# Kernel optimization log

Measured on AMD Instinct MI355X. Metric: run time of the kernel, lower is better.

## Reference

```python
import jax, jax.numpy as jnp
import numpy as np

N, EMB, ATT = 65536, 1024, 512


def setup_inputs() -> dict:
    key = jax.random.key(0)
    k = jax.random.split(key, 6)
    scale = 0.02
    return {
        "leaves": jax.random.normal(k[0], (N, EMB), dtype=jnp.float32),
        "ancestors": jax.random.normal(k[1], (N, EMB), dtype=jnp.float32),
        "W1": jax.random.normal(k[2], (2 * EMB, ATT), dtype=jnp.float32) * scale,
        "b1": jax.random.normal(k[3], (ATT,), dtype=jnp.float32) * scale,
        "W2": jax.random.normal(k[4], (ATT, 1), dtype=jnp.float32) * scale,
        "b2": jax.random.normal(k[5], (1,), dtype=jnp.float32) * scale,
    }


def reference(leaves, ancestors, W1, b1, W2, b2):
    # concat -> [N, 2*EMB]
    x = jnp.concatenate([leaves, ancestors], axis=-1)
    # additive attention MLP: linear -> tanh -> linear -> [N, 1]
    h = jnp.tanh(x @ W1 + b1)
    scores = h @ W2 + b2            # [N, 1]
    attn = jax.nn.softmax(scores, axis=0)  # softmax over the pair dim
    # reshape to [1, N], matmul ancestors [N, EMB] -> [1, EMB], sum dim 0 -> [EMB]
    out = jnp.squeeze(attn, axis=1) @ ancestors  # [EMB]
    return out
```

## Files before the change

kernel.cpp:

```cpp
#include <hip/hip_runtime.h>
#include <hip/hip_bf16.h>
#include <stdint.h>
#include <stddef.h>

typedef __bf16 bf16;
typedef bf16 bf16x8 __attribute__((ext_vector_type(8)));
typedef bf16 bf16x4 __attribute__((ext_vector_type(4)));
typedef float f32x4 __attribute__((ext_vector_type(4)));

#define N_ROWS 65536
#define EMB    1024
#define ATTD   512
#define KDIM   2048
#define BM     128
#define BK     64
#define NBLK   (N_ROWS / BM)

__device__ __forceinline__ void gload_lds16(const void* g, void* l) {
  __builtin_amdgcn_global_load_lds(
      (const __attribute__((address_space(1))) void*)g,
      (__attribute__((address_space(3))) void*)l, 16, 0, 0);
}

__global__ __launch_bounds__(256) void k_prep_w1(const float* __restrict__ W1,
                                                 bf16* __restrict__ W1t) {
  __shared__ float tile[64][65];
  const int bx = blockIdx.x;
  const int by = blockIdx.y;
  const int t  = threadIdx.x;
  const int k0 = bx * 64, n0 = by * 64;

  const int kt = t >> 2, c4 = (t & 3) * 16;
  const float* src = W1 + (size_t)(k0 + kt) * ATTD + n0 + c4;
  #pragma unroll
  for (int q = 0; q < 4; q++) {
    float4 v = *(const float4*)(src + q * 4);
    tile[kt][c4 + q * 4 + 0] = v.x;
    tile[kt][c4 + q * 4 + 1] = v.y;
    tile[kt][c4 + q * 4 + 2] = v.z;
    tile[kt][c4 + q * 4 + 3] = v.w;
  }
  __syncthreads();

  const int nr = t >> 2;
  const int n_glob = n0 + nr;
  const size_t base = (size_t)n_glob * KDIM + k0;
  #pragma unroll
  for (int h = 0; h < 2; h++) {
    const int ktbase = c4 + h * 8;
    bf16x8 o;
    #pragma unroll
    for (int e = 0; e < 8; e++) o[e] = (bf16)tile[ktbase + e][nr];
    const int chunk = ((ktbase >> 3) ^ (n_glob & 7));
    *(bf16x8*)(W1t + base + chunk * 8) = o;
  }
}

__global__ __launch_bounds__(512) void k_gemm_score(
    const float* __restrict__ leaves, const float* __restrict__ anc,
    const bf16* __restrict__ W1t, const float* __restrict__ b1,
    const float* __restrict__ W2, const float* __restrict__ b2,
    float* __restrict__ scores, float* __restrict__ bmax,
    float* __restrict__ bsum) {
  __shared__ bf16 ldsA[BM * BK];
  __shared__ bf16 ldsB[ATTD * BK];

  const int t    = threadIdx.x;
  const int lane = t & 63;
  const int wave = t >> 6;
  const int l15  = lane & 15;
  const int l4   = lane >> 4;
  const int wm   = wave >> 2;
  const int wn   = wave & 3;
  const int m0   = blockIdx.x * BM;

  const f32x4 zero4 = {0.f, 0.f, 0.f, 0.f};
  f32x4 acc[4][8];
  #pragma unroll
  for (int i = 0; i < 4; i++)
    #pragma unroll
    for (int j = 0; j < 8; j++) acc[i][j] = zero4;

  for (int kb = 0; kb < KDIM / BK; kb++) {
    const float* Abase = (kb < 16)
        ? (leaves + (size_t)m0 * EMB + (size_t)kb * BK)
        : (anc    + (size_t)m0 * EMB + (size_t)(kb - 16) * BK);
    #pragma unroll
    for (int s = 0; s < 4; s++) {
      const int i  = s * 512 + t;
      const int r  = i >> 4;
      const int c4 = i & 15;
      float4 v = *(const float4*)(Abase + (size_t)r * EMB + c4 * 4);
      bf16x4 o = {(bf16)v.x, (bf16)v.y, (bf16)v.z, (bf16)v.w};
      const int chunk = (c4 >> 1) ^ (r & 7);
      *(bf16x4*)(ldsA + r * BK + chunk * 8 + (c4 & 1) * 4) = o;
    }
    #pragma unroll
    for (int c = 0; c < 8; c++) {
      const int chunkid = (wave * 8 + c) * 64 + lane;
      const int nr = chunkid >> 3;
      const int cc = chunkid & 7;
      gload_lds16(W1t + (size_t)nr * KDIM + kb * BK + cc * 8,
                  ldsB + (wave * 8 + c) * 512);
    }
    __syncthreads();
    #pragma unroll
    for (int ks = 0; ks < 2; ks++) {
      bf16x8 afr[4];
      #pragma unroll
      for (int mi = 0; mi < 4; mi++) {
        const int row   = wm * 64 + mi * 16 + l15;
        const int chunk = (ks * 4 + l4) ^ (row & 7);
        afr[mi] = *(const bf16x8*)(ldsA + row * BK + chunk * 8);
      }
      #pragma unroll
      for (int ni = 0; ni < 8; ni++) {
        const int nrow  = wn * 128 + ni * 16 + l15;
        const int chunk = (ks * 4 + l4) ^ (nrow & 7);
        bf16x8 bfr = *(const bf16x8*)(ldsB + nrow * BK + chunk * 8);
        #pragma unroll
        for (int mi = 0; mi < 4; mi++)
          acc[mi][ni] = __builtin_amdgcn_mfma_f32_16x16x32_bf16(
              afr[mi], bfr, acc[mi][ni], 0, 0, 0);
      }
    }
    __syncthreads();
  }

  float b1c[8], w2c[8];
  #pragma unroll
  for (int ni = 0; ni < 8; ni++) {
    const int col = wn * 128 + ni * 16 + l15;
    b1c[ni] = b1[col];
    w2c[ni] = W2[col];
  }
  float* sp   = (float*)ldsA;
  float* redm = sp + 512;
  float* redz = sp + 520;
  #pragma unroll
  for (int mi = 0; mi < 4; mi++) {
    #pragma unroll
    for (int r = 0; r < 4; r++) {
      float p = 0.f;
      #pragma unroll
      for (int ni = 0; ni < 8; ni++)
        p += tanhf(acc[mi][ni][r] + b1c[ni]) * w2c[ni];
      p += __shfl_xor(p, 1);
      p += __shfl_xor(p, 2);
      p += __shfl_xor(p, 4);
      p += __shfl_xor(p, 8);
      if (l15 == 0) sp[wn * 128 + wm * 64 + mi * 16 + l4 * 4 + r] = p;
    }
  }
  __syncthreads();
  float myscore = 0.f;
  if (t < BM) {
    myscore = sp[t] + sp[128 + t] + sp[256 + t] + sp[384 + t] + b2[0];
    scores[m0 + t] = myscore;
  }
  float mm = (t < BM) ? myscore : -3.0e38f;
  #pragma unroll
  for (int o = 32; o; o >>= 1) mm = fmaxf(mm, __shfl_xor(mm, o));
  if (lane == 0) redm[wave] = mm;
  __syncthreads();
  if (t == 0) {
    float g = redm[0];
    for (int i = 1; i < 8; i++) g = fmaxf(g, redm[i]);
    redm[0] = g;
  }
  __syncthreads();
  const float bM = redm[0];
  float ee = (t < BM) ? __expf(myscore - bM) : 0.f;
  #pragma unroll
  for (int o = 32; o; o >>= 1) ee += __shfl_xor(ee, o);
  if (lane == 0) redz[wave] = ee;
  __syncthreads();
  if (t == 0) {
    float z = 0.f;
    for (int i = 0; i < 8; i++) z += redz[i];
    bmax[blockIdx.x] = bM;
    bsum[blockIdx.x] = z;
  }
}

__global__ __launch_bounds__(512) void k_mz(const float* __restrict__ bmax,
                                            const float* __restrict__ bsum,
                                            float* __restrict__ MZ) {
  const int t = threadIdx.x, lane = t & 63, wave = t >> 6;
  __shared__ float rm[8], rs[8];
  const float m = bmax[t];
  float mm = m;
  #pragma unroll
  for (int o = 32; o; o >>= 1) mm = fmaxf(mm, __shfl_xor(mm, o));
  if (lane == 0) rm[wave] = mm;
  __syncthreads();
  if (t == 0) {
    float g = rm[0];
    for (int i = 1; i < 8; i++) g = fmaxf(g, rm[i]);
    rm[0] = g;
  }
  __syncthreads();
  const float M = rm[0];
  float z = bsum[t] * __expf(m - M);
  #pragma unroll
  for (int o = 32; o; o >>= 1) z += __shfl_xor(z, o);
  if (lane == 0) rs[wave] = z;
  __syncthreads();
  if (t == 0) {
    float Z = 0.f;
    for (int i = 0; i < 8; i++) Z += rs[i];
    MZ[0] = M;
    MZ[1] = Z;
  }
}

__global__ __launch_bounds__(256) void k_part(const float* __restrict__ anc,
                                              const float* __restrict__ scores,
                                              const float* __restrict__ MZ,
                                              float* __restrict__ part) {
  __shared__ float w[BM];
  const int b = blockIdx.x, t = threadIdx.x;
  const float M = MZ[0];
  if (t < BM) w[t] = __expf(scores[(size_t)b * BM + t] - M);
  __syncthreads();
  float4 a = {0.f, 0.f, 0.f, 0.f};
  const float4* src = (const float4*)(anc + (size_t)b * BM * EMB) + t;
  #pragma unroll 4
  for (int i = 0; i < BM; i++) {
    float4 v = src[i * (EMB / 4)];
    const float wi = w[i];
    a.x += wi * v.x;
    a.y += wi * v.y;
    a.z += wi * v.z;
    a.w += wi * v.w;
  }
  ((float4*)(part + (size_t)b * EMB))[t] = a;
}

__global__ __launch_bounds__(256) void k_final(const float* __restrict__ part,
                                               const float* __restrict__ MZ,
                                               float* __restrict__ out) {
  const int j = blockIdx.x * 256 + threadIdx.x;
  float s0 = 0.f, s1 = 0.f, s2 = 0.f, s3 = 0.f;
  for (int b = 0; b < NBLK; b += 4) {
    s0 += part[(size_t)(b + 0) * EMB + j];
    s1 += part[(size_t)(b + 1) * EMB + j];
    s2 += part[(size_t)(b + 2) * EMB + j];
    s3 += part[(size_t)(b + 3) * EMB + j];
  }
  out[j] = (s0 + s1 + s2 + s3) / MZ[1];
}

extern "C" void kernel_launch(void* const* d_in, const int* in_sizes, int n_in,
                              void* d_out, int out_size, void* d_ws,
                              size_t ws_size, hipStream_t stream) {
  const float* leaves = (const float*)d_in[0];
  const float* anc    = (const float*)d_in[1];
  const float* W1     = (const float*)d_in[2];
  const float* b1     = (const float*)d_in[3];
  const float* W2     = (const float*)d_in[4];
  const float* b2     = (const float*)d_in[5];
  float* out = (float*)d_out;

  char* ws = (char*)d_ws;
  bf16*  W1t    = (bf16*)ws;
  float* scores = (float*)(ws + (1u << 21));
  float* bmax   = (float*)(ws + (1u << 21) + (1u << 18));
  float* bsum   = bmax + NBLK;
  float* MZ     = bsum + NBLK;
  float* part   = (float*)(ws + (1u << 21) + (1u << 19));

  k_prep_w1<<<dim3(32, 8), 256, 0, stream>>>(W1, W1t);
  k_gemm_score<<<dim3(NBLK), 512, 0, stream>>>(leaves, anc, W1t, b1, W2, b2,
                                               scores, bmax, bsum);
  k_mz<<<dim3(1), 512, 0, stream>>>(bmax, bsum, MZ);
  k_part<<<dim3(NBLK), 256, 0, stream>>>(anc, scores, MZ, part);
  k_final<<<dim3(EMB / 256), 256, 0, stream>>>(part, MZ, out);
}
```

Baseline: 337.6 us.

## Double-buffer GEMM LDS tiles with BK=32 and K-block-major W1 layout

Splits the K dimension into 32-wide blocks and double-buffers both A and B tiles in LDS. The next block's global loads are issued before the current MFMAs, so memory latency can overlap with compute and one barrier per iteration is dropped. The W1 prep kernel now writes a contiguous K-block-major layout with a new XOR swizzle. The trade-off is twice as many loop iterations with less MFMA work per barrier, plus extra registers held live during prefetch.

```diff
diff --git a/kernel.cpp b/kernel.cpp
--- a/kernel.cpp
+++ b/kernel.cpp
@@ -13,7 +13,8 @@
 #define ATTD   512
 #define KDIM   2048
 #define BM     128
-#define BK     64
+#define BK     32
+#define NKB    (KDIM / BK)
 #define NBLK   (N_ROWS / BM)
 
 __device__ __forceinline__ void gload_lds16(const void* g, void* l) {
@@ -24,36 +25,31 @@
 
 __global__ __launch_bounds__(256) void k_prep_w1(const float* __restrict__ W1,
                                                  bf16* __restrict__ W1t) {
-  __shared__ float tile[64][65];
-  const int bx = blockIdx.x;
-  const int by = blockIdx.y;
+  __shared__ float tile[32][72];
+  const int kb = blockIdx.x;
+  const int ng = blockIdx.y;
   const int t  = threadIdx.x;
-  const int k0 = bx * 64, n0 = by * 64;
-
-  const int kt = t >> 2, c4 = (t & 3) * 16;
-  const float* src = W1 + (size_t)(k0 + kt) * ATTD + n0 + c4;
-  #pragma unroll
-  for (int q = 0; q < 4; q++) {
-    float4 v = *(const float4*)(src + q * 4);
-    tile[kt][c4 + q * 4 + 0] = v.x;
-    tile[kt][c4 + q * 4 + 1] = v.y;
-    tile[kt][c4 + q * 4 + 2] = v.z;
-    tile[kt][c4 + q * 4 + 3] = v.w;
-  }
-  __syncthreads();
-
-  const int nr = t >> 2;
-  const int n_glob = n0 + nr;
-  const size_t base = (size_t)n_glob * KDIM + k0;
-  #pragma unroll
-  for (int h = 0; h < 2; h++) {
-    const int ktbase = c4 + h * 8;
-    bf16x8 o;
-    #pragma unroll
-    for (int e = 0; e < 8; e++) o[e] = (bf16)tile[ktbase + e][nr];
-    const int chunk = ((ktbase >> 3) ^ (n_glob & 7));
-    *(bf16x8*)(W1t + base + chunk * 8) = o;
-  }
+  const int n0 = ng * 64;
+
+  const int kr  = t >> 3;
+  const int nc8 = (t & 7) * 8;
+  const float* src = W1 + (size_t)(kb * 32 + kr) * ATTD + n0 + nc8;
+  float4 v0 = *(const float4*)(src);
+  float4 v1 = *(const float4*)(src + 4);
+  tile[kr][nc8 + 0] = v0.x; tile[kr][nc8 + 1] = v0.y;
+  tile[kr][nc8 + 2] = v0.z; tile[kr][nc8 + 3] = v0.w;
+  tile[kr][nc8 + 4] = v1.x; tile[kr][nc8 + 5] = v1.y;
+  tile[kr][nc8 + 6] = v1.z; tile[kr][nc8 + 7] = v1.w;
+  __syncthreads();
+
+  const int nl = t >> 2;
+  const int p  = t & 3;
+  const int n  = n0 + nl;
+  const int c  = p ^ ((n >> 1) & 3);
+  bf16x8 o;
+  #pragma unroll
+  for (int e = 0; e < 8; e++) o[e] = (bf16)tile[c * 8 + e][nl];
+  *(bf16x8*)(W1t + (size_t)kb * (ATTD * BK) + (size_t)n * 32 + p * 8) = o;
 }
 
 __global__ __launch_bounds__(512) void k_gemm_score(
@@ -62,8 +58,8 @@
     const float* __restrict__ W2, const float* __restrict__ b2,
     float* __restrict__ scores, float* __restrict__ bmax,
     float* __restrict__ bsum) {
-  __shared__ bf16 ldsA[BM * BK];
-  __shared__ bf16 ldsB[ATTD * BK];
+  __shared__ bf16 ldsA[2][BM * BK];
+  __shared__ bf16 ldsB[2][ATTD * BK];
 
   const int t    = threadIdx.x;
   const int lane = t & 63;
@@ -74,6 +70,11 @@
   const int wn   = wave & 3;
   const int m0   = blockIdx.x * BM;
 
+  const int ar = t >> 2;
+  const int ac = t & 3;
+  const int apc = ac ^ ((ar >> 1) & 3);
+  const int a_lds_off = ar * BK + apc * 8;
+
   const f32x4 zero4 = {0.f, 0.f, 0.f, 0.f};
   f32x4 acc[4][8];
   #pragma unroll
@@ -81,48 +82,66 @@
     #pragma unroll
     for (int j = 0; j < 8; j++) acc[i][j] = zero4;
 
-  for (int kb = 0; kb < KDIM / BK; kb++) {
-    const float* Abase = (kb < 16)
-        ? (leaves + (size_t)m0 * EMB + (size_t)kb * BK)
-        : (anc    + (size_t)m0 * EMB + (size_t)(kb - 16) * BK);
-    #pragma unroll
-    for (int s = 0; s < 4; s++) {
-      const int i  = s * 512 + t;
-      const int r  = i >> 4;
-      const int c4 = i & 15;
-      float4 v = *(const float4*)(Abase + (size_t)r * EMB + c4 * 4);
-      bf16x4 o = {(bf16)v.x, (bf16)v.y, (bf16)v.z, (bf16)v.w};
-      const int chunk = (c4 >> 1) ^ (r & 7);
-      *(bf16x4*)(ldsA + r * BK + chunk * 8 + (c4 & 1) * 4) = o;
-    }
-    #pragma unroll
-    for (int c = 0; c < 8; c++) {
-      const int chunkid = (wave * 8 + c) * 64 + lane;
-      const int nr = chunkid >> 3;
-      const int cc = chunkid & 7;
-      gload_lds16(W1t + (size_t)nr * KDIM + kb * BK + cc * 8,
-                  ldsB + (wave * 8 + c) * 512);
-    }
+  int a_rd[4];
+  #pragma unroll
+  for (int mi = 0; mi < 4; mi++) {
+    const int row = wm * 64 + mi * 16 + l15;
+    a_rd[mi] = row * BK + (l4 ^ ((row >> 1) & 3)) * 8;
+  }
+  int b_rd[8];
+  #pragma unroll
+  for (int ni = 0; ni < 8; ni++) {
+    const int nrow = wn * 128 + ni * 16 + l15;
+    b_rd[ni] = nrow * BK + (l4 ^ ((nrow >> 1) & 3)) * 8;
+  }
+
+  {
+    const float* Abase = leaves + (size_t)m0 * EMB;
+    float4 v0 = *(const float4*)(Abase + (size_t)ar * EMB + ac * 8);
+    float4 v1 = *(const float4*)(Abase + (size_t)ar * EMB + ac * 8 + 4);
+    #pragma unroll
+    for (int j = 0; j < 4; j++)
+      gload_lds16(W1t + ((size_t)(wave * 4 + j) * 64 + lane) * 8,
+                  &ldsB[0][(wave * 4 + j) * 512]);
+    bf16x8 o = {(bf16)v0.x, (bf16)v0.y, (bf16)v0.z, (bf16)v0.w,
+                (bf16)v1.x, (bf16)v1.y, (bf16)v1.z, (bf16)v1.w};
+    *(bf16x8*)(&ldsA[0][a_lds_off]) = o;
     __syncthreads();
-    #pragma unroll
-    for (int ks = 0; ks < 2; ks++) {
-      bf16x8 afr[4];
+  }
+
+  for (int kb = 0; kb < NKB; kb++) {
+    const int cur = kb & 1, nxt = cur ^ 1;
+    float4 v0, v1;
+    const bool pf = (kb < NKB - 1);
+    if (pf) {
+      const int kn = kb + 1;
+      const float* Abase = (kn < 32)
+          ? (leaves + (size_t)m0 * EMB + (size_t)kn * BK)
+          : (anc    + (size_t)m0 * EMB + (size_t)(kn - 32) * BK);
+      v0 = *(const float4*)(Abase + (size_t)ar * EMB + ac * 8);
+      v1 = *(const float4*)(Abase + (size_t)ar * EMB + ac * 8 + 4);
+      const bf16* Bsrc = W1t + (size_t)kn * (ATTD * BK);
       #pragma unroll
-      for (int mi = 0; mi < 4; mi++) {
-        const int row   = wm * 64 + mi * 16 + l15;
-        const int chunk = (ks * 4 + l4) ^ (row & 7);
-        afr[mi] = *(const bf16x8*)(ldsA + row * BK + chunk * 8);
-      }
+      for (int j = 0; j < 4; j++)
+        gload_lds16(Bsrc + ((size_t)(wave * 4 + j) * 64 + lane) * 8,
+                    &ldsB[nxt][(wave * 4 + j) * 512]);
+    }
+    bf16x8 afr[4];
+    #pragma unroll
+    for (int mi = 0; mi < 4; mi++)
+      afr[mi] = *(const bf16x8*)(&ldsA[cur][a_rd[mi]]);
+    #pragma unroll
+    for (int ni = 0; ni < 8; ni++) {
+      bf16x8 bfr = *(const bf16x8*)(&ldsB[cur][b_rd[ni]]);
       #pragma unroll
-      for (int ni = 0; ni < 8; ni++) {
-        const int nrow  = wn * 128 + ni * 16 + l15;
-        const int chunk = (ks * 4 + l4) ^ (nrow & 7);
-        bf16x8 bfr = *(const bf16x8*)(ldsB + nrow * BK + chunk * 8);
-        #pragma unroll
-        for (int mi = 0; mi < 4; mi++)
-          acc[mi][ni] = __builtin_amdgcn_mfma_f32_16x16x32_bf16(
-              afr[mi], bfr, acc[mi][ni], 0, 0, 0);
-      }
+      for (int mi = 0; mi < 4; mi++)
+        acc[mi][ni] = __builtin_amdgcn_mfma_f32_16x16x32_bf16(
+            afr[mi], bfr, acc[mi][ni], 0, 0, 0);
+    }
+    if (pf) {
+      bf16x8 o = {(bf16)v0.x, (bf16)v0.y, (bf16)v0.z, (bf16)v0.w,
+                  (bf16)v1.x, (bf16)v1.y, (bf16)v1.z, (bf16)v1.w};
+      *(bf16x8*)(&ldsA[nxt][a_lds_off]) = o;
     }
     __syncthreads();
   }
@@ -134,7 +153,7 @@
     b1c[ni] = b1[col];
     w2c[ni] = W2[col];
   }
-  float* sp   = (float*)ldsA;
+  float* sp   = (float*)&ldsA[0][0];
   float* redm = sp + 512;
   float* redz = sp + 520;
   #pragma unroll
@@ -270,7 +289,7 @@
   float* MZ     = bsum + NBLK;
   float* part   = (float*)(ws + (1u << 21) + (1u << 19));
 
-  k_prep_w1<<<dim3(32, 8), 256, 0, stream>>>(W1, W1t);
+  k_prep_w1<<<dim3(64, 8), 256, 0, stream>>>(W1, W1t);
   k_gemm_score<<<dim3(NBLK), 512, 0, stream>>>(leaves, anc, W1t, b1, W2, b2,
                                                scores, bmax, bsum);
   k_mz<<<dim3(1), 512, 0, stream>>>(bmax, bsum, MZ);
```

Measured after the change: 361.2 us. 7.0% more time.

## Double-buffer GEMM LDS tiles with register-prefetched A and k-block-major W1 layout

Applied to the files above, without the earlier changes.

Reworks the score GEMM into a software pipeline: LDS A and B tiles are double-buffered, A for k-block kb+2 is prefetched into registers while block kb computes, and W1 for the next block is streamed via global_load_lds into the alternate buffer, with a single manual waitcnt+barrier per step instead of two syncthreads. W1t is re-laid out k-block-major so each block's B tile is one contiguous 64KB chunk. Launch bounds request 2 blocks per CU. This trades doubled LDS (160KB per block) and higher register pressure for overlap of loads with MFMA; LDS size may actually limit occupancy to one block.

```diff
diff --git a/kernel.cpp b/kernel.cpp
--- a/kernel.cpp
+++ b/kernel.cpp
@@ -5,7 +5,6 @@
 
 typedef __bf16 bf16;
 typedef bf16 bf16x8 __attribute__((ext_vector_type(8)));
-typedef bf16 bf16x4 __attribute__((ext_vector_type(4)));
 typedef float f32x4 __attribute__((ext_vector_type(4)));
 
 #define N_ROWS 65536
@@ -14,6 +13,7 @@
 #define KDIM   2048
 #define BM     128
 #define BK     64
+#define NKB    (KDIM / BK)
 #define NBLK   (N_ROWS / BM)
 
 __device__ __forceinline__ void gload_lds16(const void* g, void* l) {
@@ -24,46 +24,46 @@
 
 __global__ __launch_bounds__(256) void k_prep_w1(const float* __restrict__ W1,
                                                  bf16* __restrict__ W1t) {
-  __shared__ float tile[64][65];
-  const int bx = blockIdx.x;
-  const int by = blockIdx.y;
+  __shared__ float tile[64][72];
+  const int kb = blockIdx.x;
+  const int ng = blockIdx.y;
   const int t  = threadIdx.x;
-  const int k0 = bx * 64, n0 = by * 64;
-
-  const int kt = t >> 2, c4 = (t & 3) * 16;
-  const float* src = W1 + (size_t)(k0 + kt) * ATTD + n0 + c4;
-  #pragma unroll
-  for (int q = 0; q < 4; q++) {
+  const int n0 = ng * 64;
+
+  const int kr = t >> 2;
+  const int nc = (t & 3) * 16;
+  const float* src = W1 + (size_t)(kb * 64 + kr) * ATTD + n0 + nc;
+  #pragma unroll
+  for (int q = 0; q < 4; ++q) {
     float4 v = *(const float4*)(src + q * 4);
-    tile[kt][c4 + q * 4 + 0] = v.x;
-    tile[kt][c4 + q * 4 + 1] = v.y;
-    tile[kt][c4 + q * 4 + 2] = v.z;
-    tile[kt][c4 + q * 4 + 3] = v.w;
-  }
-  __syncthreads();
-
-  const int nr = t >> 2;
-  const int n_glob = n0 + nr;
-  const size_t base = (size_t)n_glob * KDIM + k0;
-  #pragma unroll
-  for (int h = 0; h < 2; h++) {
-    const int ktbase = c4 + h * 8;
+    tile[kr][nc + q * 4 + 0] = v.x;
+    tile[kr][nc + q * 4 + 1] = v.y;
+    tile[kr][nc + q * 4 + 2] = v.z;
+    tile[kr][nc + q * 4 + 3] = v.w;
+  }
+  __syncthreads();
+
+  const int nl = t >> 2;
+  const int n  = n0 + nl;
+  #pragma unroll
+  for (int h = 0; h < 2; ++h) {
+    const int p = (t & 3) + h * 4;
+    const int c = p ^ (n & 7);
     bf16x8 o;
     #pragma unroll
-    for (int e = 0; e < 8; e++) o[e] = (bf16)tile[ktbase + e][nr];
-    const int chunk = ((ktbase >> 3) ^ (n_glob & 7));
-    *(bf16x8*)(W1t + base + chunk * 8) = o;
-  }
-}
-
-__global__ __launch_bounds__(512) void k_gemm_score(
+    for (int e = 0; e < 8; ++e) o[e] = (bf16)tile[c * 8 + e][nl];
+    *(bf16x8*)(W1t + (size_t)kb * (ATTD * BK) + ((size_t)n * 8 + p) * 8) = o;
+  }
+}
+
+__global__ __launch_bounds__(512, 2) void k_gemm_score(
     const float* __restrict__ leaves, const float* __restrict__ anc,
     const bf16* __restrict__ W1t, const float* __restrict__ b1,
     const float* __restrict__ W2, const float* __restrict__ b2,
     float* __restrict__ scores, float* __restrict__ bmax,
     float* __restrict__ bsum) {
-  __shared__ bf16 ldsA[BM * BK];
-  __shared__ bf16 ldsB[ATTD * BK];
+  __shared__ bf16 ldsA[2][BM * BK];
+  __shared__ bf16 ldsB[2][ATTD * BK];
 
   const int t    = threadIdx.x;
   const int lane = t & 63;
@@ -74,76 +74,132 @@
   const int wn   = wave & 3;
   const int m0   = blockIdx.x * BM;
 
+  const int ar  = t >> 2;
+  const int acb = (t & 3) * 2;
+
   const f32x4 zero4 = {0.f, 0.f, 0.f, 0.f};
   f32x4 acc[4][8];
   #pragma unroll
-  for (int i = 0; i < 4; i++)
+  for (int i = 0; i < 4; ++i)
     #pragma unroll
-    for (int j = 0; j < 8; j++) acc[i][j] = zero4;
-
-  for (int kb = 0; kb < KDIM / BK; kb++) {
-    const float* Abase = (kb < 16)
-        ? (leaves + (size_t)m0 * EMB + (size_t)kb * BK)
-        : (anc    + (size_t)m0 * EMB + (size_t)(kb - 16) * BK);
+    for (int j = 0; j < 8; ++j) acc[i][j] = zero4;
+
+  float4 rA0[4], rA1[4];
+
+  {
+    const float* Ap0 = leaves + (size_t)(m0 + ar) * EMB + acb * 8;
+    rA0[0] = *(const float4*)(Ap0 + 0);
+    rA0[1] = *(const float4*)(Ap0 + 4);
+    rA0[2] = *(const float4*)(Ap0 + 8);
+    rA0[3] = *(const float4*)(Ap0 + 12);
     #pragma unroll
-    for (int s = 0; s < 4; s++) {
-      const int i  = s * 512 + t;
-      const int r  = i >> 4;
-      const int c4 = i & 15;
-      float4 v = *(const float4*)(Abase + (size_t)r * EMB + c4 * 4);
-      bf16x4 o = {(bf16)v.x, (bf16)v.y, (bf16)v.z, (bf16)v.w};
-      const int chunk = (c4 >> 1) ^ (r & 7);
-      *(bf16x4*)(ldsA + r * BK + chunk * 8 + (c4 & 1) * 4) = o;
-    }
-    #pragma unroll
-    for (int c = 0; c < 8; c++) {
-      const int chunkid = (wave * 8 + c) * 64 + lane;
-      const int nr = chunkid >> 3;
-      const int cc = chunkid & 7;
-      gload_lds16(W1t + (size_t)nr * KDIM + kb * BK + cc * 8,
-                  ldsB + (wave * 8 + c) * 512);
-    }
-    __syncthreads();
-    #pragma unroll
-    for (int ks = 0; ks < 2; ks++) {
-      bf16x8 afr[4];
-      #pragma unroll
-      for (int mi = 0; mi < 4; mi++) {
-        const int row   = wm * 64 + mi * 16 + l15;
-        const int chunk = (ks * 4 + l4) ^ (row & 7);
-        afr[mi] = *(const bf16x8*)(ldsA + row * BK + chunk * 8);
-      }
-      #pragma unroll
-      for (int ni = 0; ni < 8; ni++) {
-        const int nrow  = wn * 128 + ni * 16 + l15;
-        const int chunk = (ks * 4 + l4) ^ (nrow & 7);
-        bf16x8 bfr = *(const bf16x8*)(ldsB + nrow * BK + chunk * 8);
-        #pragma unroll
-        for (int mi = 0; mi < 4; mi++)
-          acc[mi][ni] = __builtin_amdgcn_mfma_f32_16x16x32_bf16(
-              afr[mi], bfr, acc[mi][ni], 0, 0, 0);
-      }
-    }
-    __syncthreads();
-  }
+    for (int j = 0; j < 8; ++j)
+      gload_lds16(W1t + ((size_t)(wave * 8 + j) * 64 + lane) * 8,
+                  &ldsB[0][(wave * 8 + j) * 512]);
+    const float* Ap1 = leaves + (size_t)(m0 + ar) * EMB + BK + acb * 8;
+    rA1[0] = *(const float4*)(Ap1 + 0);
+    rA1[1] = *(const float4*)(Ap1 + 4);
+    rA1[2] = *(const float4*)(Ap1 + 8);
+    rA1[3] = *(const float4*)(Ap1 + 12);
+    __builtin_amdgcn_sched_barrier(0);
+    bf16x8 o0 = {(bf16)rA0[0].x, (bf16)rA0[0].y, (bf16)rA0[0].z, (bf16)rA0[0].w,
+                 (bf16)rA0[1].x, (bf16)rA0[1].y, (bf16)rA0[1].z, (bf16)rA0[1].w};
+    bf16x8 o1 = {(bf16)rA0[2].x, (bf16)rA0[2].y, (bf16)rA0[2].z, (bf16)rA0[2].w,
+                 (bf16)rA0[3].x, (bf16)rA0[3].y, (bf16)rA0[3].z, (bf16)rA0[3].w};
+    *(bf16x8*)(&ldsA[0][ar * BK + ((acb + 0) ^ (ar & 7)) * 8]) = o0;
+    *(bf16x8*)(&ldsA[0][ar * BK + ((acb + 1) ^ (ar & 7)) * 8]) = o1;
+    asm volatile("s_waitcnt vmcnt(4) lgkmcnt(0)" ::: "memory");
+    __builtin_amdgcn_s_barrier();
+  }
+
+#define GEMM_BODY(KB, CUR, RISS, RWR, DOSTAGE, DOAISS)                         \
+  do {                                                                         \
+    if (DOSTAGE) {                                                             \
+      const bf16* Bsrc_ = W1t + (size_t)((KB) + 1) * (ATTD * BK);              \
+      _Pragma("unroll")                                                        \
+      for (int j = 0; j < 8; ++j)                                              \
+        gload_lds16(Bsrc_ + ((size_t)(wave * 8 + j) * 64 + lane) * 8,          \
+                    &ldsB[(CUR) ^ 1][(wave * 8 + j) * 512]);                   \
+      if (DOAISS) {                                                            \
+        const int kn_ = (KB) + 2;                                              \
+        const float* Ap_ = (kn_ < 16)                                          \
+            ? leaves + (size_t)(m0 + ar) * EMB + (size_t)kn_ * BK + acb * 8    \
+            : anc + (size_t)(m0 + ar) * EMB + (size_t)(kn_ - 16) * BK + acb * 8;\
+        RISS[0] = *(const float4*)(Ap_ + 0);                                   \
+        RISS[1] = *(const float4*)(Ap_ + 4);                                   \
+        RISS[2] = *(const float4*)(Ap_ + 8);                                   \
+        RISS[3] = *(const float4*)(Ap_ + 12);                                  \
+      }                                                                        \
+      __builtin_amdgcn_sched_barrier(0);                                       \
+    }                                                                          \
+    _Pragma("unroll")                                                          \
+    for (int ks = 0; ks < 2; ++ks) {                                           \
+      bf16x8 af_[4], bf_[8];                                                   \
+      _Pragma("unroll")                                                        \
+      for (int mi = 0; mi < 4; ++mi) {                                         \
+        const int row_ = wm * 64 + mi * 16 + l15;                              \
+        const int p_   = (ks * 4 + l4) ^ (row_ & 7);                           \
+        af_[mi] = *(const bf16x8*)(&ldsA[CUR][row_ * BK + p_ * 8]);            \
+      }                                                                        \
+      _Pragma("unroll")                                                        \
+      for (int ni = 0; ni < 8; ++ni) {                                         \
+        const int nrow_ = wn * 128 + ni * 16 + l15;                            \
+        const int p_    = (ks * 4 + l4) ^ (nrow_ & 7);                         \
+        bf_[ni] = *(const bf16x8*)(&ldsB[CUR][nrow_ * BK + p_ * 8]);           \
+      }                                                                        \
+      _Pragma("unroll")                                                        \
+      for (int ni = 0; ni < 8; ++ni)                                           \
+        _Pragma("unroll")                                                      \
+        for (int mi = 0; mi < 4; ++mi)                                         \
+          acc[mi][ni] = __builtin_amdgcn_mfma_f32_16x16x32_bf16(               \
+              af_[mi], bf_[ni], acc[mi][ni], 0, 0, 0);                         \
+    }                                                                          \
+    if (DOSTAGE) {                                                             \
+      bf16x8 w0_ = {(bf16)RWR[0].x, (bf16)RWR[0].y, (bf16)RWR[0].z,            \
+                    (bf16)RWR[0].w, (bf16)RWR[1].x, (bf16)RWR[1].y,            \
+                    (bf16)RWR[1].z, (bf16)RWR[1].w};                           \
+      bf16x8 w1_ = {(bf16)RWR[2].x, (bf16)RWR[2].y, (bf16)RWR[2].z,            \
+                    (bf16)RWR[2].w, (bf16)RWR[3].x, (bf16)RWR[3].y,            \
+                    (bf16)RWR[3].z, (bf16)RWR[3].w};                           \
+      *(bf16x8*)(&ldsA[(CUR) ^ 1][ar * BK + ((acb + 0) ^ (ar & 7)) * 8]) = w0_;\
+      *(bf16x8*)(&ldsA[(CUR) ^ 1][ar * BK + ((acb + 1) ^ (ar & 7)) * 8]) = w1_;\
+      if (DOAISS) {                                                            \
+        asm volatile("s_waitcnt vmcnt(4) lgkmcnt(0)" ::: "memory");            \
+      } else {                                                                 \
+        asm volatile("s_waitcnt vmcnt(0) lgkmcnt(0)" ::: "memory");            \
+      }                                                                        \
+    } else {                                                                   \
+      asm volatile("s_waitcnt lgkmcnt(0)" ::: "memory");                       \
+    }                                                                          \
+    __builtin_amdgcn_s_barrier();                                              \
+  } while (0)
+
+  for (int kbp = 0; kbp < 15; ++kbp) {
+    const int kb = kbp * 2;
+    GEMM_BODY(kb,     0, rA0, rA1, true, true);
+    GEMM_BODY(kb + 1, 1, rA1, rA0, true, true);
+  }
+  GEMM_BODY(30, 0, rA0, rA1, true,  false);
+  GEMM_BODY(31, 1, rA0, rA1, false, false);
+#undef GEMM_BODY
 
   float b1c[8], w2c[8];
   #pragma unroll
-  for (int ni = 0; ni < 8; ni++) {
+  for (int ni = 0; ni < 8; ++ni) {
     const int col = wn * 128 + ni * 16 + l15;
     b1c[ni] = b1[col];
     w2c[ni] = W2[col];
   }
-  float* sp   = (float*)ldsA;
+  float* sp   = (float*)&ldsA[0][0];
   float* redm = sp + 512;
   float* redz = sp + 520;
   #pragma unroll
-  for (int mi = 0; mi < 4; mi++) {
+  for (int mi = 0; mi < 4; ++mi) {
     #pragma unroll
-    for (int r = 0; r < 4; r++) {
+    for (int r = 0; r < 4; ++r) {
       float p = 0.f;
       #pragma unroll
-      for (int ni = 0; ni < 8; ni++)
+      for (int ni = 0; ni < 8; ++ni)
         p += tanhf(acc[mi][ni][r] + b1c[ni]) * w2c[ni];
       p += __shfl_xor(p, 1);
       p += __shfl_xor(p, 2);
@@ -165,7 +221,7 @@
   __syncthreads();
   if (t == 0) {
     float g = redm[0];
-    for (int i = 1; i < 8; i++) g = fmaxf(g, redm[i]);
+    for (int i = 1; i < 8; ++i) g = fmaxf(g, redm[i]);
     redm[0] = g;
   }
   __syncthreads();
@@ -177,7 +233,7 @@
   __syncthreads();
   if (t == 0) {
     float z = 0.f;
-    for (int i = 0; i < 8; i++) z += redz[i];
+    for (int i = 0; i < 8; ++i) z += redz[i];
     bmax[blockIdx.x] = bM;
     bsum[blockIdx.x] = z;
   }
@@ -196,7 +252,7 @@
   __syncthreads();
   if (t == 0) {
     float g = rm[0];
-    for (int i = 1; i < 8; i++) g = fmaxf(g, rm[i]);
+    for (int i = 1; i < 8; ++i) g = fmaxf(g, rm[i]);
     rm[0] = g;
   }
   __syncthreads();
@@ -208,7 +264,7 @@
   __syncthreads();
   if (t == 0) {
     float Z = 0.f;
-    for (int i = 0; i < 8; i++) Z += rs[i];
+    for (int i = 0; i < 8; ++i) Z += rs[i];
     MZ[0] = M;
     MZ[1] = Z;
   }
@@ -226,7 +282,7 @@
   float4 a = {0.f, 0.f, 0.f, 0.f};
   const float4* src = (const float4*)(anc + (size_t)b * BM * EMB) + t;
   #pragma unroll 4
-  for (int i = 0; i < BM; i++) {
+  for (int i = 0; i < BM; ++i) {
     float4 v = src[i * (EMB / 4)];
     const float wi = w[i];
     a.x += wi * v.x;
```

Result: slower. 505.8 us (+49.8%).

## Split GEMM over N into 128-wide tiles and reorganize softmax reduction pipeline

Applied to the files above, without the earlier changes.

The GEMM block now covers 128x128 tiles with 256 threads instead of 128x512 with 512 threads, so there are four times as many blocks and more can be resident at once. W1 is pre-packed into contiguous per-tile bf16 blocks so the B loads into LDS are contiguous. Partial scores from the four N-splits are written out and summed in a new combine kernel. k_part now weights with per-block maxima and k_final rescales each block, so k_part no longer waits on the global max. The cost is that each A tile (fp32 activations) is read and converted four times, once per N-split.

```diff
diff --git a/kernel.cpp b/kernel.cpp
--- a/kernel.cpp
+++ b/kernel.cpp
@@ -5,7 +5,6 @@
 
 typedef __bf16 bf16;
 typedef bf16 bf16x8 __attribute__((ext_vector_type(8)));
-typedef bf16 bf16x4 __attribute__((ext_vector_type(4)));
 typedef float f32x4 __attribute__((ext_vector_type(4)));
 
 #define N_ROWS 65536
@@ -13,8 +12,11 @@
 #define ATTD   512
 #define KDIM   2048
 #define BM     128
+#define BN     128
 #define BK     64
-#define NBLK   (N_ROWS / BM)
+#define NKB    (KDIM / BK)
+#define MBLK   (N_ROWS / BM)
+#define NSPL   (ATTD / BN)
 
 __device__ __forceinline__ void gload_lds16(const void* g, void* l) {
   __builtin_amdgcn_global_load_lds(
@@ -24,168 +26,186 @@
 
 __global__ __launch_bounds__(256) void k_prep_w1(const float* __restrict__ W1,
                                                  bf16* __restrict__ W1t) {
-  __shared__ float tile[64][65];
-  const int bx = blockIdx.x;
-  const int by = blockIdx.y;
+  __shared__ float tile[64][132];
+  const int kb = blockIdx.x;
+  const int bn = blockIdx.y;
   const int t  = threadIdx.x;
-  const int k0 = bx * 64, n0 = by * 64;
-
-  const int kt = t >> 2, c4 = (t & 3) * 16;
-  const float* src = W1 + (size_t)(k0 + kt) * ATTD + n0 + c4;
-  #pragma unroll
-  for (int q = 0; q < 4; q++) {
+
+  const int kr = t >> 2;
+  const int nc = (t & 3) * 32;
+  const float* src = W1 + (size_t)(kb * 64 + kr) * ATTD + bn * 128 + nc;
+  #pragma unroll
+  for (int q = 0; q < 8; ++q) {
     float4 v = *(const float4*)(src + q * 4);
-    tile[kt][c4 + q * 4 + 0] = v.x;
-    tile[kt][c4 + q * 4 + 1] = v.y;
-    tile[kt][c4 + q * 4 + 2] = v.z;
-    tile[kt][c4 + q * 4 + 3] = v.w;
-  }
-  __syncthreads();
-
-  const int nr = t >> 2;
-  const int n_glob = n0 + nr;
-  const size_t base = (size_t)n_glob * KDIM + k0;
-  #pragma unroll
-  for (int h = 0; h < 2; h++) {
-    const int ktbase = c4 + h * 8;
+    tile[kr][nc + q * 4 + 0] = v.x;
+    tile[kr][nc + q * 4 + 1] = v.y;
+    tile[kr][nc + q * 4 + 2] = v.z;
+    tile[kr][nc + q * 4 + 3] = v.w;
+  }
+  __syncthreads();
+
+  const int nl = t >> 1;
+  const int pb = (t & 1) * 4;
+  bf16* dst = W1t + (size_t)(kb * 4 + bn) * (BN * BK);
+  #pragma unroll
+  for (int pi = 0; pi < 4; ++pi) {
+    const int p = pb + pi;
+    const int c = p ^ (nl & 7);
     bf16x8 o;
     #pragma unroll
-    for (int e = 0; e < 8; e++) o[e] = (bf16)tile[ktbase + e][nr];
-    const int chunk = ((ktbase >> 3) ^ (n_glob & 7));
-    *(bf16x8*)(W1t + base + chunk * 8) = o;
-  }
-}
-
-__global__ __launch_bounds__(512) void k_gemm_score(
+    for (int e = 0; e < 8; ++e) o[e] = (bf16)tile[c * 8 + e][nl];
+    *(bf16x8*)(dst + ((size_t)nl * 8 + p) * 8) = o;
+  }
+}
+
+__global__ __launch_bounds__(256, 3) void k_gemm_score(
     const float* __restrict__ leaves, const float* __restrict__ anc,
     const bf16* __restrict__ W1t, const float* __restrict__ b1,
-    const float* __restrict__ W2, const float* __restrict__ b2,
-    float* __restrict__ scores, float* __restrict__ bmax,
-    float* __restrict__ bsum) {
+    const float* __restrict__ W2, float* __restrict__ spart) {
   __shared__ bf16 ldsA[BM * BK];
-  __shared__ bf16 ldsB[ATTD * BK];
+  __shared__ bf16 ldsB[BN * BK];
 
   const int t    = threadIdx.x;
   const int lane = t & 63;
   const int wave = t >> 6;
   const int l15  = lane & 15;
   const int l4   = lane >> 4;
-  const int wm   = wave >> 2;
-  const int wn   = wave & 3;
-  const int m0   = blockIdx.x * BM;
+  const int wm2  = wave >> 1;
+  const int wn2  = wave & 1;
+  const int bn   = blockIdx.x & 3;
+  const int bm   = blockIdx.x >> 2;
+  const int m0   = bm * BM;
+  const int n0   = bn * BN;
+
+  const int ar   = t >> 1;
+  const int half = t & 1;
 
   const f32x4 zero4 = {0.f, 0.f, 0.f, 0.f};
-  f32x4 acc[4][8];
-  #pragma unroll
-  for (int i = 0; i < 4; i++)
-    #pragma unroll
-    for (int j = 0; j < 8; j++) acc[i][j] = zero4;
-
-  for (int kb = 0; kb < KDIM / BK; kb++) {
-    const float* Abase = (kb < 16)
-        ? (leaves + (size_t)m0 * EMB + (size_t)kb * BK)
-        : (anc    + (size_t)m0 * EMB + (size_t)(kb - 16) * BK);
-    #pragma unroll
-    for (int s = 0; s < 4; s++) {
-      const int i  = s * 512 + t;
-      const int r  = i >> 4;
-      const int c4 = i & 15;
-      float4 v = *(const float4*)(Abase + (size_t)r * EMB + c4 * 4);
-      bf16x4 o = {(bf16)v.x, (bf16)v.y, (bf16)v.z, (bf16)v.w};
-      const int chunk = (c4 >> 1) ^ (r & 7);
-      *(bf16x4*)(ldsA + r * BK + chunk * 8 + (c4 & 1) * 4) = o;
-    }
-    #pragma unroll
-    for (int c = 0; c < 8; c++) {
-      const int chunkid = (wave * 8 + c) * 64 + lane;
-      const int nr = chunkid >> 3;
-      const int cc = chunkid & 7;
-      gload_lds16(W1t + (size_t)nr * KDIM + kb * BK + cc * 8,
-                  ldsB + (wave * 8 + c) * 512);
+  f32x4 acc[4][4];
+  #pragma unroll
+  for (int i = 0; i < 4; ++i)
+    #pragma unroll
+    for (int j = 0; j < 4; ++j) acc[i][j] = zero4;
+
+  for (int kb = 0; kb < NKB; ++kb) {
+    const bf16* Bsrc = W1t + (size_t)(kb * 4 + bn) * (BN * BK);
+    #pragma unroll
+    for (int j = 0; j < 4; ++j)
+      gload_lds16(Bsrc + ((size_t)(wave * 4 + j) * 64 + lane) * 8,
+                  ldsB + (wave * 4 + j) * 512);
+    const float* Ap = ((kb < 16)
+        ? leaves + (size_t)(m0 + ar) * EMB + (size_t)kb * BK
+        : anc    + (size_t)(m0 + ar) * EMB + (size_t)(kb - 16) * BK)
+        + half * 32;
+    float4 v0 = *(const float4*)(Ap + 0);
+    float4 v1 = *(const float4*)(Ap + 4);
+    float4 v2 = *(const float4*)(Ap + 8);
+    float4 v3 = *(const float4*)(Ap + 12);
+    float4 v4 = *(const float4*)(Ap + 16);
+    float4 v5 = *(const float4*)(Ap + 20);
+    float4 v6 = *(const float4*)(Ap + 24);
+    float4 v7 = *(const float4*)(Ap + 28);
+    {
+      bf16x8 o0 = {(bf16)v0.x, (bf16)v0.y, (bf16)v0.z, (bf16)v0.w,
+                   (bf16)v1.x, (bf16)v1.y, (bf16)v1.z, (bf16)v1.w};
+      bf16x8 o1 = {(bf16)v2.x, (bf16)v2.y, (bf16)v2.z, (bf16)v2.w,
+                   (bf16)v3.x, (bf16)v3.y, (bf16)v3.z, (bf16)v3.w};
+      bf16x8 o2 = {(bf16)v4.x, (bf16)v4.y, (bf16)v4.z, (bf16)v4.w,
+                   (bf16)v5.x, (bf16)v5.y, (bf16)v5.z, (bf16)v5.w};
+      bf16x8 o3 = {(bf16)v6.x, (bf16)v6.y, (bf16)v6.z, (bf16)v6.w,
+                   (bf16)v7.x, (bf16)v7.y, (bf16)v7.z, (bf16)v7.w};
+      const int c0 = half * 4;
+      *(bf16x8*)(ldsA + ar * BK + ((c0 + 0) ^ (ar & 7)) * 8) = o0;
+      *(bf16x8*)(ldsA + ar * BK + ((c0 + 1) ^ (ar & 7)) * 8) = o1;
+      *(bf16x8*)(ldsA + ar * BK + ((c0 + 2) ^ (ar & 7)) * 8) = o2;
+      *(bf16x8*)(ldsA + ar * BK + ((c0 + 3) ^ (ar & 7)) * 8) = o3;
     }
     __syncthreads();
     #pragma unroll
-    for (int ks = 0; ks < 2; ks++) {
-      bf16x8 afr[4];
+    for (int ks = 0; ks < 2; ++ks) {
+      bf16x8 af[4], bfr[4];
       #pragma unroll
-      for (int mi = 0; mi < 4; mi++) {
-        const int row   = wm * 64 + mi * 16 + l15;
-        const int chunk = (ks * 4 + l4) ^ (row & 7);
-        afr[mi] = *(const bf16x8*)(ldsA + row * BK + chunk * 8);
+      for (int mi = 0; mi < 4; ++mi) {
+        const int row = wm2 * 64 + mi * 16 + l15;
+        const int p   = (ks * 4 + l4) ^ (row & 7);
+        af[mi] = *(const bf16x8*)(ldsA + row * BK + p * 8);
       }
       #pragma unroll
-      for (int ni = 0; ni < 8; ni++) {
-        const int nrow  = wn * 128 + ni * 16 + l15;
-        const int chunk = (ks * 4 + l4) ^ (nrow & 7);
-        bf16x8 bfr = *(const bf16x8*)(ldsB + nrow * BK + chunk * 8);
+      for (int ni = 0; ni < 4; ++ni) {
+        const int nrow = wn2 * 64 + ni * 16 + l15;
+        const int p    = (ks * 4 + l4) ^ (nrow & 7);
+        bfr[ni] = *(const bf16x8*)(ldsB + nrow * BK + p * 8);
+      }
+      #pragma unroll
+      for (int ni = 0; ni < 4; ++ni)
         #pragma unroll
-        for (int mi = 0; mi < 4; mi++)
+        for (int mi = 0; mi < 4; ++mi)
           acc[mi][ni] = __builtin_amdgcn_mfma_f32_16x16x32_bf16(
-              afr[mi], bfr, acc[mi][ni], 0, 0, 0);
-      }
+              af[mi], bfr[ni], acc[mi][ni], 0, 0, 0);
     }
     __syncthreads();
   }
 
-  float b1c[8], w2c[8];
-  #pragma unroll
-  for (int ni = 0; ni < 8; ni++) {
-    const int col = wn * 128 + ni * 16 + l15;
+  float b1c[4], w2c[4];
+  #pragma unroll
+  for (int ni = 0; ni < 4; ++ni) {
+    const int col = n0 + wn2 * 64 + ni * 16 + l15;
     b1c[ni] = b1[col];
     w2c[ni] = W2[col];
   }
-  float* sp   = (float*)ldsA;
-  float* redm = sp + 512;
-  float* redz = sp + 520;
-  #pragma unroll
-  for (int mi = 0; mi < 4; mi++) {
-    #pragma unroll
-    for (int r = 0; r < 4; r++) {
+  float* sp = (float*)ldsA;
+  #pragma unroll
+  for (int mi = 0; mi < 4; ++mi) {
+    #pragma unroll
+    for (int r = 0; r < 4; ++r) {
       float p = 0.f;
       #pragma unroll
-      for (int ni = 0; ni < 8; ni++)
+      for (int ni = 0; ni < 4; ++ni)
         p += tanhf(acc[mi][ni][r] + b1c[ni]) * w2c[ni];
       p += __shfl_xor(p, 1);
       p += __shfl_xor(p, 2);
       p += __shfl_xor(p, 4);
       p += __shfl_xor(p, 8);
-      if (l15 == 0) sp[wn * 128 + wm * 64 + mi * 16 + l4 * 4 + r] = p;
+      if (l15 == 0) sp[wn2 * 128 + wm2 * 64 + mi * 16 + l4 * 4 + r] = p;
     }
   }
   __syncthreads();
-  float myscore = 0.f;
-  if (t < BM) {
-    myscore = sp[t] + sp[128 + t] + sp[256 + t] + sp[384 + t] + b2[0];
-    scores[m0 + t] = myscore;
-  }
-  float mm = (t < BM) ? myscore : -3.0e38f;
+  if (t < BM)
+    spart[(size_t)bn * N_ROWS + m0 + t] = sp[t] + sp[128 + t];
+}
+
+__global__ __launch_bounds__(128) void k_combine(
+    const float* __restrict__ spart, const float* __restrict__ b2,
+    float* __restrict__ scores, float* __restrict__ bmax,
+    float* __restrict__ bsum) {
+  const int b = blockIdx.x, t = threadIdx.x;
+  const int lane = t & 63, wave = t >> 6;
+  const int m = b * 128 + t;
+  __shared__ float rm[2], rs[2];
+  const float s = spart[m] + spart[N_ROWS + m] + spart[2 * N_ROWS + m] +
+                  spart[3 * N_ROWS + m] + b2[0];
+  scores[m] = s;
+  float mm = s;
   #pragma unroll
   for (int o = 32; o; o >>= 1) mm = fmaxf(mm, __shfl_xor(mm, o));
-  if (lane == 0) redm[wave] = mm;
+  if (lane == 0) rm[wave] = mm;
+  __syncthreads();
+  const float bM = fmaxf(rm[0], rm[1]);
+  float ee = __expf(s - bM);
+  #pragma unroll
+  for (int o = 32; o; o >>= 1) ee += __shfl_xor(ee, o);
+  if (lane == 0) rs[wave] = ee;
   __syncthreads();
   if (t == 0) {
-    float g = redm[0];
-    for (int i = 1; i < 8; i++) g = fmaxf(g, redm[i]);
-    redm[0] = g;
-  }
-  __syncthreads();
-  const float bM = redm[0];
-  float ee = (t < BM) ? __expf(myscore - bM) : 0.f;
-  #pragma unroll
-  for (int o = 32; o; o >>= 1) ee += __shfl_xor(ee, o);
-  if (lane == 0) redz[wave] = ee;
-  __syncthreads();
-  if (t == 0) {
-    float z = 0.f;
-    for (int i = 0; i < 8; i++) z += redz[i];
-    bmax[blockIdx.x] = bM;
-    bsum[blockIdx.x] = z;
+    bmax[b] = bM;
+    bsum[b] = rs[0] + rs[1];
   }
 }
 
 __global__ __launch_bounds__(512) void k_mz(const float* __restrict__ bmax,
                                             const float* __restrict__ bsum,
-                                            float* __restrict__ MZ) {
+                                            float* __restrict__ MZ,
+                                            float* __restrict__ scale) {
   const int t = threadIdx.x, lane = t & 63, wave = t >> 6;
   __shared__ float rm[8], rs[8];
   const float m = bmax[t];
@@ -196,19 +216,21 @@
   __syncthreads();
   if (t == 0) {
     float g = rm[0];
-    for (int i = 1; i < 8; i++) g = fmaxf(g, rm[i]);
+    for (int i = 1; i < 8; ++i) g = fmaxf(g, rm[i]);
     rm[0] = g;
   }
   __syncthreads();
   const float M = rm[0];
-  float z = bsum[t] * __expf(m - M);
+  const float sc = __expf(m - M);
+  scale[t] = sc;
+  float z = bsum[t] * sc;
   #pragma unroll
   for (int o = 32; o; o >>= 1) z += __shfl_xor(z, o);
   if (lane == 0) rs[wave] = z;
   __syncthreads();
   if (t == 0) {
     float Z = 0.f;
-    for (int i = 0; i < 8; i++) Z += rs[i];
+    for (int i = 0; i < 8; ++i) Z += rs[i];
     MZ[0] = M;
     MZ[1] = Z;
   }
@@ -216,17 +238,17 @@
 
 __global__ __launch_bounds__(256) void k_part(const float* __restrict__ anc,
                                               const float* __restrict__ scores,
-                                              const float* __restrict__ MZ,
+                                              const float* __restrict__ bmax,
                                               float* __restrict__ part) {
   __shared__ float w[BM];
   const int b = blockIdx.x, t = threadIdx.x;
-  const float M = MZ[0];
-  if (t < BM) w[t] = __expf(scores[(size_t)b * BM + t] - M);
+  const float bM = bmax[b];
+  if (t < BM) w[t] = __expf(scores[(size_t)b * BM + t] - bM);
   __syncthreads();
   float4 a = {0.f, 0.f, 0.f, 0.f};
   const float4* src = (const float4*)(anc + (size_t)b * BM * EMB) + t;
   #pragma unroll 4
-  for (int i = 0; i < BM; i++) {
+  for (int i = 0; i < BM; ++i) {
     float4 v = src[i * (EMB / 4)];
     const float wi = w[i];
     a.x += wi * v.x;
@@ -238,15 +260,16 @@
 }
 
 __global__ __launch_bounds__(256) void k_final(const float* __restrict__ part,
+                                               const float* __restrict__ scale,
                                                const float* __restrict__ MZ,
                                                float* __restrict__ out) {
   const int j = blockIdx.x * 256 + threadIdx.x;
   float s0 = 0.f, s1 = 0.f, s2 = 0.f, s3 = 0.f;
-  for (int b = 0; b < NBLK; b += 4) {
-    s0 += part[(size_t)(b + 0) * EMB + j];
-    s1 += part[(size_t)(b + 1) * EMB + j];
-    s2 += part[(size_t)(b + 2) * EMB + j];
-    s3 += part[(size_t)(b + 3) * EMB + j];
+  for (int b = 0; b < MBLK; b += 4) {
+    s0 += part[(size_t)(b + 0) * EMB + j] * scale[b + 0];
+    s1 += part[(size_t)(b + 1) * EMB + j] * scale[b + 1];
+    s2 += part[(size_t)(b + 2) * EMB + j] * scale[b + 2];
+    s3 += part[(size_t)(b + 3) * EMB + j] * scale[b + 3];
   }
   out[j] = (s0 + s1 + s2 + s3) / MZ[1];
 }
@@ -264,16 +287,19 @@
 
   char* ws = (char*)d_ws;
   bf16*  W1t    = (bf16*)ws;
-  float* scores = (float*)(ws + (1u << 21));
-  float* bmax   = (float*)(ws + (1u << 21) + (1u << 18));
-  float* bsum   = bmax + NBLK;
-  float* MZ     = bsum + NBLK;
-  float* part   = (float*)(ws + (1u << 21) + (1u << 19));
-
-  k_prep_w1<<<dim3(32, 8), 256, 0, stream>>>(W1, W1t);
-  k_gemm_score<<<dim3(NBLK), 512, 0, stream>>>(leaves, anc, W1t, b1, W2, b2,
-                                               scores, bmax, bsum);
-  k_mz<<<dim3(1), 512, 0, stream>>>(bmax, bsum, MZ);
-  k_part<<<dim3(NBLK), 256, 0, stream>>>(anc, scores, MZ, part);
-  k_final<<<dim3(EMB / 256), 256, 0, stream>>>(part, MZ, out);
-}
+  float* spart  = (float*)(ws + (2u << 20));
+  float* scores = (float*)(ws + (3u << 20));
+  float* bmax   = (float*)(ws + (3u << 20) + (1u << 18));
+  float* bsum   = bmax + MBLK;
+  float* scale  = bsum + MBLK;
+  float* MZ     = scale + MBLK;
+  float* part   = (float*)(ws + (4u << 20));
+
+  k_prep_w1<<<dim3(32, 4), 256, 0, stream>>>(W1, W1t);
+  k_gemm_score<<<dim3(MBLK * NSPL), 256, 0, stream>>>(leaves, anc, W1t, b1, W2,
+                                                      spart);
+  k_combine<<<dim3(MBLK), 128, 0, stream>>>(spart, b2, scores, bmax, bsum);
+  k_mz<<<dim3(1), 512, 0, stream>>>(bmax, bsum, MZ, scale);
+  k_part<<<dim3(MBLK), 256, 0, stream>>>(anc, scores, bmax, part);
+  k_final<<<dim3(EMB / 256), 256, 0, stream>>>(part, scale, MZ, out);
+}
```

Measured after the change: 410.3 us. 21.5% more time.
